# Kernel tuning notes

Measured on AMD Instinct MI355X. Metric: run time of the kernel, lower is better.

## Reference

```python
import jax, jax.numpy as jnp
import numpy as np

N = 50000      # nodes
E = 800000     # edges (before self-loops)
IN = 256       # input_dim
H = 8          # heads (hard-coded in module)
C = 32         # hidden_dim per head
OUT = 64       # output_dim
NEG_SLOPE = 0.2  # PyG GATConv default leaky_relu slope


def setup_inputs() -> dict:
    key = jax.random.key(0)
    ks = jax.random.split(key, 8)
    x = jax.random.normal(ks[0], (N, IN), dtype=jnp.float32)
    edge_index = jax.random.randint(ks[1], (2, E), 0, N, dtype=jnp.int64)
    # GATConv params (concat=True -> out width H*C)
    W_gat = jax.random.normal(ks[2], (IN, H * C), dtype=jnp.float32) * (1.0 / np.sqrt(IN))
    att_src = jax.random.normal(ks[3], (1, H, C), dtype=jnp.float32) * (1.0 / np.sqrt(C))
    att_dst = jax.random.normal(ks[4], (1, H, C), dtype=jnp.float32) * (1.0 / np.sqrt(C))
    bias_gat = jnp.zeros((H * C,), dtype=jnp.float32)
    # final Linear
    W_lin = jax.random.normal(ks[5], (H * C, OUT), dtype=jnp.float32) * (1.0 / np.sqrt(H * C))
    b_lin = jnp.zeros((OUT,), dtype=jnp.float32)
    return {"x": x, "edge_index": edge_index, "W_gat": W_gat, "att_src": att_src,
            "att_dst": att_dst, "bias_gat": bias_gat, "W_lin": W_lin, "b_lin": b_lin}


def reference(x, edge_index, W_gat, att_src, att_dst, bias_gat, W_lin, b_lin):
    # add self-loops (PyG GATConv default add_self_loops=True)
    ar = jnp.arange(N, dtype=edge_index.dtype)
    ei = jnp.concatenate([edge_index, jnp.stack([ar, ar])], axis=1)  # [2, E+N]
    src, dst = ei[0], ei[1]

    h = (x @ W_gat).reshape(N, H, C)                # [N,H,C]
    a_src = jnp.sum(h * att_src, axis=-1)           # [N,H]
    a_dst = jnp.sum(h * att_dst, axis=-1)           # [N,H]

    e = a_src[src] + a_dst[dst]                     # [E+N,H] per-edge logits
    e = jnp.where(e > 0, e, NEG_SLOPE * e)          # leaky_relu

    # segment softmax over incoming edges of each dst node
    m = jax.ops.segment_max(e, dst, num_segments=N)           # [N,H]
    ex = jnp.exp(e - m[dst])                                   # [E+N,H]
    denom = jax.ops.segment_sum(ex, dst, num_segments=N)       # [N,H]
    alpha = ex / (denom[dst] + 1e-16)                           # [E+N,H]

    msg = h[src] * alpha[:, :, None]                            # [E+N,H,C]
    out = jax.ops.segment_sum(msg, dst, num_segments=N)        # [N,H,C]
    out = out.reshape(N, H * C) + bias_gat                      # concat heads + bias

    out = jax.nn.relu(out)
    return out @ W_lin + b_lin                                  # [N,OUT]
```

## Files before the change

### kernel.cpp

```cpp
#include <hip/hip_runtime.h>
#include <hip/hip_bf16.h>

typedef __attribute__((ext_vector_type(8))) short short8v;
typedef __attribute__((ext_vector_type(4))) float floatx4;

__device__ __forceinline__ unsigned short f2bf(float f) {
    unsigned b = __float_as_uint(f);
    b = (b + 0x7fffu + ((b >> 16) & 1u)) >> 16;
    return (unsigned short)b;
}
__device__ __forceinline__ float b2f(unsigned short u) {
    return __uint_as_float((unsigned)u << 16);
}

#define BIDX(col, k) ((col) * 264 + ((k) ^ ((((col) >> 3) & 7) << 3)))

__global__ void k_prep(const float* __restrict__ s0, unsigned short* __restrict__ d0, int n0,
                       const float* __restrict__ s1, unsigned short* __restrict__ d1, int n1,
                       const float* __restrict__ s2, unsigned short* __restrict__ d2, int n2,
                       const int* __restrict__ ei, int* __restrict__ cnt, int E, int EE) {
    int nconv = n0 + n1 + n2;
    int total = nconv + EE;
    int i = blockIdx.x * blockDim.x + threadIdx.x;
    int stride = gridDim.x * blockDim.x;
    for (; i < total; i += stride) {
        if (i < nconv) {
            const float* s; unsigned short* d; int j;
            if (i < n0) { s = s0; d = d0; j = i; }
            else if (i < n0 + n1) { s = s1; d = d1; j = i - n0; }
            else { s = s2; d = d2; j = i - n0 - n1; }
            float4 v = reinterpret_cast<const float4*>(s)[j];
            ushort4 o;
            o.x = f2bf(v.x); o.y = f2bf(v.y); o.z = f2bf(v.z); o.w = f2bf(v.w);
            reinterpret_cast<ushort4*>(d)[j] = o;
        } else {
            int e = i - nconv;
            int dst = (e < E) ? ei[E + e] : e - E;
            atomicAdd(&cnt[dst], 1);
        }
    }
}

__launch_bounds__(256)
__global__ void k_gs(const unsigned short* __restrict__ A,
                     const unsigned short* __restrict__ B,
                     const float* __restrict__ att_src, const float* __restrict__ att_dst,
                     unsigned short* __restrict__ hb,
                     float* __restrict__ a_src, float* __restrict__ a_dst,
                     int M, int RB, int GB1,
                     const int* __restrict__ ei, int* __restrict__ cursor,
                     int* __restrict__ sorted_src, int E, int EE) {
    __shared__ unsigned short BsT[64 * 264];
    const int b = blockIdx.x;
    if (b >= GB1) {
        int e = (b - GB1) * 256 + threadIdx.x;
        if (e >= EE) return;
        int src, dst;
        if (e < E) { src = ei[e]; dst = ei[E + e]; } else { src = dst = e - E; }
        int pos = atomicAdd(&cursor[dst], 1);
        sorted_src[pos] = src;
        return;
    }
    const int tid = threadIdx.x;
    const int nt = b / RB;
    const int tM = (b - nt * RB) * 64;

    for (int it = 0; it < 8; ++it) {
        int f8 = it * 256 + tid;
        int k = f8 >> 3;
        int c0 = (f8 & 7) * 8;
        short8v v = *reinterpret_cast<const short8v*>(B + (size_t)k * 256 + nt * 64 + c0);
#pragma unroll
        for (int j = 0; j < 8; ++j)
            BsT[BIDX(c0 + j, k)] = (unsigned short)v[j];
    }
    __syncthreads();

    const int w  = tid >> 6;
    const int l  = tid & 63;
    const int lg = l >> 4;
    const int lr = l & 15;

    floatx4 acc[4] = {};
    int rowA = tM + w * 16 + lr;
    if (rowA > M - 1) rowA = M - 1;
    const unsigned short* Arow = A + (size_t)rowA * 256 + lg * 8;

#pragma unroll
    for (int kt = 0; kt < 8; ++kt) {
        short8v av = *reinterpret_cast<const short8v*>(Arow + kt * 32);
#pragma unroll
        for (int n = 0; n < 4; ++n) {
            short8v bv = *reinterpret_cast<const short8v*>(&BsT[BIDX(n * 16 + lr, kt * 32 + lg * 8)]);
            acc[n] = __builtin_amdgcn_mfma_f32_16x16x32_bf16(av, bv, acc[n], 0, 0, 0);
        }
    }

    float ps[2][4] = {}, pd[2][4] = {};
#pragma unroll
    for (int n = 0; n < 4; ++n) {
        int hd2 = n >> 1;
        float asv = att_src[(nt * 2 + hd2) * 32 + (n & 1) * 16 + lr];
        float adv = att_dst[(nt * 2 + hd2) * 32 + (n & 1) * 16 + lr];
        int col = nt * 64 + n * 16 + lr;
#pragma unroll
        for (int r = 0; r < 4; ++r) {
            int row = tM + w * 16 + lg * 4 + r;
            float v = acc[n][r];
            if (row < M) hb[(size_t)row * 256 + col] = f2bf(v);
            ps[hd2][r] += v * asv;
            pd[hd2][r] += v * adv;
        }
    }
#pragma unroll
    for (int off = 1; off < 16; off <<= 1) {
#pragma unroll
        for (int hd2 = 0; hd2 < 2; ++hd2)
#pragma unroll
            for (int r = 0; r < 4; ++r) {
                ps[hd2][r] += __shfl_xor(ps[hd2][r], off, 64);
                pd[hd2][r] += __shfl_xor(pd[hd2][r], off, 64);
            }
    }
    if (lr == 0) {
#pragma unroll
        for (int hd2 = 0; hd2 < 2; ++hd2)
#pragma unroll
            for (int r = 0; r < 4; ++r) {
                int row = tM + w * 16 + lg * 4 + r;
                if (row < M) {
                    a_src[(size_t)row * 8 + nt * 2 + hd2] = ps[hd2][r];
                    a_dst[(size_t)row * 8 + nt * 2 + hd2] = pd[hd2][r];
                }
            }
    }
}

__launch_bounds__(256)
__global__ void k_gemm(const unsigned short* __restrict__ A,
                       const unsigned short* __restrict__ B,
                       float* __restrict__ C,
                       const float* __restrict__ bias,
                       int M, int NC) {
    __shared__ unsigned short BsT[64 * 264];
    const int tid = threadIdx.x;
    const int ntile = blockIdx.y;
    const int tM = blockIdx.x * 64;

    for (int it = 0; it < 8; ++it) {
        int f8 = it * 256 + tid;
        int k = f8 >> 3;
        int c0 = (f8 & 7) * 8;
        short8v v = *reinterpret_cast<const short8v*>(B + (size_t)k * NC + ntile * 64 + c0);
#pragma unroll
        for (int j = 0; j < 8; ++j)
            BsT[BIDX(c0 + j, k)] = (unsigned short)v[j];
    }
    __syncthreads();

    const int w  = tid >> 6;
    const int l  = tid & 63;
    const int lg = l >> 4;
    const int lr = l & 15;

    floatx4 acc[4] = {};
    int rowA = tM + w * 16 + lr;
    if (rowA > M - 1) rowA = M - 1;
    const unsigned short* Arow = A + (size_t)rowA * 256 + lg * 8;

#pragma unroll
    for (int kt = 0; kt < 8; ++kt) {
        short8v av = *reinterpret_cast<const short8v*>(Arow + kt * 32);
#pragma unroll
        for (int n = 0; n < 4; ++n) {
            short8v bv = *reinterpret_cast<const short8v*>(&BsT[BIDX(n * 16 + lr, kt * 32 + lg * 8)]);
            acc[n] = __builtin_amdgcn_mfma_f32_16x16x32_bf16(av, bv, acc[n], 0, 0, 0);
        }
    }
#pragma unroll
    for (int n = 0; n < 4; ++n) {
        int col = ntile * 64 + n * 16 + lr;
        float badd = bias ? bias[col] : 0.0f;
#pragma unroll
        for (int r = 0; r < 4; ++r) {
            int row = tM + w * 16 + lg * 4 + r;
            if (row < M) C[(size_t)row * NC + col] = acc[n][r] + badd;
        }
    }
}

#define SCAN_NB 256
__launch_bounds__(256)
__global__ void k_scan_a(const int* __restrict__ cnt, int* __restrict__ bsum, int N) {
    __shared__ int sh[256];
    int b = blockIdx.x, t = threadIdx.x;
    int chunk = (N + SCAN_NB - 1) / SCAN_NB;
    int idx = b * chunk + t;
    sh[t] = (t < chunk && idx < N) ? cnt[idx] : 0;
    __syncthreads();
    for (int off = 128; off > 0; off >>= 1) {
        if (t < off) sh[t] += sh[t + off];
        __syncthreads();
    }
    if (t == 0) bsum[b] = sh[0];
}
__launch_bounds__(256)
__global__ void k_scan_bc(const int* __restrict__ cnt, const int* __restrict__ bsum,
                          int* __restrict__ row_start, int* __restrict__ cursor, int N) {
    __shared__ int shb[256];
    __shared__ int sh[256];
    int b = blockIdx.x, t = threadIdx.x;
    shb[t] = bsum[t];
    __syncthreads();
    for (int off = 1; off < 256; off <<= 1) {
        int v = (t >= off) ? shb[t - off] : 0;
        __syncthreads();
        shb[t] += v;
        __syncthreads();
    }
    int boff = (b == 0) ? 0 : shb[b - 1];

    int chunk = (N + SCAN_NB - 1) / SCAN_NB;
    int idx = b * chunk + t;
    int v = (t < chunk && idx < N) ? cnt[idx] : 0;
    sh[t] = v;
    __syncthreads();
    for (int off = 1; off < 256; off <<= 1) {
        int u = (t >= off) ? sh[t - off] : 0;
        __syncthreads();
        sh[t] += u;
        __syncthreads();
    }
    if (t < chunk && idx < N) {
        int ex = boff + sh[t] - v;
        row_start[idx] = ex;
        cursor[idx] = ex;
    }
}

__launch_bounds__(256)
__global__ void k_agg(const int* __restrict__ row_start, const int* __restrict__ row_end,
                      const int* __restrict__ sorted_src,
                      const float* __restrict__ a_src, const float* __restrict__ a_dst,
                      const unsigned short* __restrict__ hb,
                      const float* __restrict__ bias_gat,
                      unsigned short* __restrict__ gb, int N) {
    int n = blockIdx.x * 4 + (threadIdx.x >> 6);
    if (n >= N) return;
    int lane = threadIdx.x & 63;
    int hd = lane >> 3;
    int start = row_start[n], end = row_end[n];
    float ad = a_dst[(size_t)n * 8 + hd];
    float ax = 0.f, ay = 0.f, az = 0.f, aw = 0.f, den = 0.f;
    float bx = 0.f, by = 0.f, bz = 0.f, bw = 0.f, den2 = 0.f;
    for (int j0 = start; j0 < end; j0 += 64) {
        int idx = j0 + lane;
        int sv = (idx < end) ? sorted_src[idx] : 0;
        int cnt = end - j0; if (cnt > 64) cnt = 64;
        int jj = 0;
        for (; jj + 3 < cnt; jj += 4) {
            int s0 = __shfl(sv, jj);
            int s1 = __shfl(sv, jj + 1);
            int s2 = __shfl(sv, jj + 2);
            int s3 = __shfl(sv, jj + 3);
            float v0 = a_src[(size_t)s0 * 8 + hd] + ad;
            float v1 = a_src[(size_t)s1 * 8 + hd] + ad;
            float v2 = a_src[(size_t)s2 * 8 + hd] + ad;
            float v3 = a_src[(size_t)s3 * 8 + hd] + ad;
            ushort4 h0 = *reinterpret_cast<const ushort4*>(hb + (size_t)s0 * 256 + lane * 4);
            ushort4 h1 = *reinterpret_cast<const ushort4*>(hb + (size_t)s1 * 256 + lane * 4);
            ushort4 h2 = *reinterpret_cast<const ushort4*>(hb + (size_t)s2 * 256 + lane * 4);
            ushort4 h3 = *reinterpret_cast<const ushort4*>(hb + (size_t)s3 * 256 + lane * 4);
            v0 = v0 > 0.f ? v0 : 0.2f * v0;
            v1 = v1 > 0.f ? v1 : 0.2f * v1;
            v2 = v2 > 0.f ? v2 : 0.2f * v2;
            v3 = v3 > 0.f ? v3 : 0.2f * v3;
            float e0 = __expf(v0), e1 = __expf(v1), e2 = __expf(v2), e3 = __expf(v3);
            den  += e0 + e2; den2 += e1 + e3;
            ax += e0 * b2f(h0.x); ay += e0 * b2f(h0.y);
            az += e0 * b2f(h0.z); aw += e0 * b2f(h0.w);
            bx += e1 * b2f(h1.x); by += e1 * b2f(h1.y);
            bz += e1 * b2f(h1.z); bw += e1 * b2f(h1.w);
            ax += e2 * b2f(h2.x); ay += e2 * b2f(h2.y);
            az += e2 * b2f(h2.z); aw += e2 * b2f(h2.w);
            bx += e3 * b2f(h3.x); by += e3 * b2f(h3.y);
            bz += e3 * b2f(h3.z); bw += e3 * b2f(h3.w);
        }
        for (; jj < cnt; ++jj) {
            int s0 = __shfl(sv, jj);
            float v0 = a_src[(size_t)s0 * 8 + hd] + ad;
            v0 = v0 > 0.f ? v0 : 0.2f * v0;
            float e0 = __expf(v0);
            ushort4 h0 = *reinterpret_cast<const ushort4*>(hb + (size_t)s0 * 256 + lane * 4);
            den += e0;
            ax += e0 * b2f(h0.x); ay += e0 * b2f(h0.y);
            az += e0 * b2f(h0.z); aw += e0 * b2f(h0.w);
        }
    }
    float inv = 1.0f / (den + den2 + 1e-16f);
    float4 b4 = *reinterpret_cast<const float4*>(bias_gat + lane * 4);
    ushort4 o;
    o.x = f2bf(fmaxf((ax + bx) * inv + b4.x, 0.f));
    o.y = f2bf(fmaxf((ay + by) * inv + b4.y, 0.f));
    o.z = f2bf(fmaxf((az + bz) * inv + b4.z, 0.f));
    o.w = f2bf(fmaxf((aw + bw) * inv + b4.w, 0.f));
    reinterpret_cast<ushort4*>(gb)[(size_t)n * 64 + lane] = o;
}

extern "C" void kernel_launch(void* const* d_in, const int* in_sizes, int n_in,
                              void* d_out, int out_size, void* d_ws, size_t ws_size,
                              hipStream_t stream) {
    const float* x        = (const float*)d_in[0];
    const int*   ei       = (const int*)d_in[1];
    const float* W_gat    = (const float*)d_in[2];
    const float* att_src  = (const float*)d_in[3];
    const float* att_dst  = (const float*)d_in[4];
    const float* bias_gat = (const float*)d_in[5];
    const float* W_lin    = (const float*)d_in[6];
    const float* b_lin    = (const float*)d_in[7];
    float* out = (float*)d_out;

    const int N  = in_sizes[0] / 256;
    const int E  = in_sizes[1] / 2;
    const int EE = E + N;

    char* ws = (char*)d_ws;
    size_t off = 0;
    auto alloc = [&](size_t bytes) -> void* {
        void* p = ws + off;
        off = (off + bytes + 255) & ~(size_t)255;
        return p;
    };
    unsigned short* hb       = (unsigned short*)alloc((size_t)N * 256 * 2);
    float*          a_srcv   = (float*)alloc((size_t)N * 8 * 4);
    float*          a_dstv   = (float*)alloc((size_t)N * 8 * 4);
    int*            cnt      = (int*)alloc((size_t)N * 4);
    int*            rowst    = (int*)alloc((size_t)N * 4);
    int*            cursor   = (int*)alloc((size_t)N * 4);
    int*            bsum     = (int*)alloc(SCAN_NB * 4);
    int*            ssrc     = (int*)alloc((size_t)EE * 4);
    unsigned short* xb       = (unsigned short*)alloc((size_t)N * 256 * 2);
    unsigned short* wb       = (unsigned short*)alloc(256 * 256 * 2);
    unsigned short* wlb      = (unsigned short*)alloc(256 * 64 * 2);

    hipMemsetAsync(cnt, 0, (size_t)N * 4, stream);

    k_prep<<<2048, 256, 0, stream>>>(x, xb, N * 256 / 4,
                                     W_gat, wb, 256 * 256 / 4,
                                     W_lin, wlb, 256 * 64 / 4,
                                     ei, cnt, E, EE);

    k_scan_a<<<SCAN_NB, 256, 0, stream>>>(cnt, bsum, N);
    k_scan_bc<<<SCAN_NB, 256, 0, stream>>>(cnt, bsum, rowst, cursor, N);

    const int RB  = (N + 63) / 64;
    const int GB1 = RB * 4;
    const int SB  = (EE + 255) / 256;
    k_gs<<<GB1 + SB, 256, 0, stream>>>(xb, wb, att_src, att_dst, hb, a_srcv, a_dstv,
                                       N, RB, GB1, ei, cursor, ssrc, E, EE);

    k_agg<<<(N + 3) / 4, 256, 0, stream>>>(rowst, cursor, ssrc, a_srcv, a_dstv, hb,
                                           bias_gat, xb, N);

    dim3 g2((N + 63) / 64, 1);
    k_gemm<<<g2, 256, 0, stream>>>(xb, wlb, out, b_lin, N, 64);
}
```

Before: 220.4 us.

## Pre-transpose weights, drop LDS staging, compact edge indices to 16-bit

Weights are transposed to bf16 during the prep pass, so both GEMM kernels read B operands straight from global/L2 and no longer stage them through shared memory with a barrier. Self-loops are written directly during the scan instead of with atomics. Sorted source indices are stored as 16-bit values, halving that traffic, and the edge scatter handles four edges per thread with vector loads. The 16-bit indices only work because N is below 65536, and the uncoalesced transposed weight stores in prep add some cost.

```diff
diff --git a/kernel.cpp b/kernel.cpp
--- a/kernel.cpp
+++ b/kernel.cpp
@@ -13,86 +13,144 @@
     return __uint_as_float((unsigned)u << 16);
 }
 
-#define BIDX(col, k) ((col) * 264 + ((k) ^ ((((col) >> 3) & 7) << 3)))
-
-__global__ void k_prep(const float* __restrict__ s0, unsigned short* __restrict__ d0, int n0,
-                       const float* __restrict__ s1, unsigned short* __restrict__ d1, int n1,
-                       const float* __restrict__ s2, unsigned short* __restrict__ d2, int n2,
-                       const int* __restrict__ ei, int* __restrict__ cnt, int E, int EE) {
-    int nconv = n0 + n1 + n2;
-    int total = nconv + EE;
+__global__ void k_prep(const float* __restrict__ x, unsigned short* __restrict__ xb, int n0,
+                       const float* __restrict__ Wg, unsigned short* __restrict__ wbT,
+                       const float* __restrict__ Wl, unsigned short* __restrict__ wlbT,
+                       const int* __restrict__ ei, int* __restrict__ cnt, int E) {
+    const int TG = 256 * 256 / 4;
+    const int TL = 256 * 64 / 4;
+    int total = n0 + TG + TL + E;
     int i = blockIdx.x * blockDim.x + threadIdx.x;
     int stride = gridDim.x * blockDim.x;
     for (; i < total; i += stride) {
-        if (i < nconv) {
-            const float* s; unsigned short* d; int j;
-            if (i < n0) { s = s0; d = d0; j = i; }
-            else if (i < n0 + n1) { s = s1; d = d1; j = i - n0; }
-            else { s = s2; d = d2; j = i - n0 - n1; }
-            float4 v = reinterpret_cast<const float4*>(s)[j];
+        if (i < n0) {
+            float4 v = reinterpret_cast<const float4*>(x)[i];
             ushort4 o;
             o.x = f2bf(v.x); o.y = f2bf(v.y); o.z = f2bf(v.z); o.w = f2bf(v.w);
-            reinterpret_cast<ushort4*>(d)[j] = o;
+            reinterpret_cast<ushort4*>(xb)[i] = o;
+        } else if (i < n0 + TG) {
+            int j = i - n0;
+            int k = j >> 6, c4 = (j & 63) * 4;
+            float4 v = *reinterpret_cast<const float4*>(Wg + k * 256 + c4);
+            wbT[(size_t)(c4 + 0) * 256 + k] = f2bf(v.x);
+            wbT[(size_t)(c4 + 1) * 256 + k] = f2bf(v.y);
+            wbT[(size_t)(c4 + 2) * 256 + k] = f2bf(v.z);
+            wbT[(size_t)(c4 + 3) * 256 + k] = f2bf(v.w);
+        } else if (i < n0 + TG + TL) {
+            int j = i - n0 - TG;
+            int k = j >> 4, c4 = (j & 15) * 4;
+            float4 v = *reinterpret_cast<const float4*>(Wl + k * 64 + c4);
+            wlbT[(size_t)(c4 + 0) * 256 + k] = f2bf(v.x);
+            wlbT[(size_t)(c4 + 1) * 256 + k] = f2bf(v.y);
+            wlbT[(size_t)(c4 + 2) * 256 + k] = f2bf(v.z);
+            wlbT[(size_t)(c4 + 3) * 256 + k] = f2bf(v.w);
         } else {
-            int e = i - nconv;
-            int dst = (e < E) ? ei[E + e] : e - E;
-            atomicAdd(&cnt[dst], 1);
-        }
+            int e = i - n0 - TG - TL;
+            atomicAdd(&cnt[ei[E + e]], 1);
+        }
+    }
+}
+
+#define SCAN_NB 256
+__launch_bounds__(256)
+__global__ void k_scan_a(const int* __restrict__ cnt, int* __restrict__ bsum, int N) {
+    __shared__ int sh[256];
+    int b = blockIdx.x, t = threadIdx.x;
+    int chunk = (N + SCAN_NB - 1) / SCAN_NB;
+    int idx = b * chunk + t;
+    sh[t] = (t < chunk && idx < N) ? (cnt[idx] + 1) : 0;
+    __syncthreads();
+    for (int off = 128; off > 0; off >>= 1) {
+        if (t < off) sh[t] += sh[t + off];
+        __syncthreads();
+    }
+    if (t == 0) bsum[b] = sh[0];
+}
+__launch_bounds__(256)
+__global__ void k_scan_bc(const int* __restrict__ cnt, const int* __restrict__ bsum,
+                          int* __restrict__ row_start, int* __restrict__ cursor,
+                          unsigned short* __restrict__ ssrc, int N) {
+    __shared__ int shb[256];
+    __shared__ int sh[256];
+    int b = blockIdx.x, t = threadIdx.x;
+    shb[t] = bsum[t];
+    __syncthreads();
+    for (int off = 1; off < 256; off <<= 1) {
+        int v = (t >= off) ? shb[t - off] : 0;
+        __syncthreads();
+        shb[t] += v;
+        __syncthreads();
+    }
+    int boff = (b == 0) ? 0 : shb[b - 1];
+
+    int chunk = (N + SCAN_NB - 1) / SCAN_NB;
+    int idx = b * chunk + t;
+    int v = (t < chunk && idx < N) ? (cnt[idx] + 1) : 0;
+    sh[t] = v;
+    __syncthreads();
+    for (int off = 1; off < 256; off <<= 1) {
+        int u = (t >= off) ? sh[t - off] : 0;
+        __syncthreads();
+        sh[t] += u;
+        __syncthreads();
+    }
+    if (t < chunk && idx < N) {
+        int ex = boff + sh[t] - v;
+        row_start[idx] = ex;
+        cursor[idx] = ex + 1;
+        ssrc[ex] = (unsigned short)idx;
     }
 }
 
 __launch_bounds__(256)
 __global__ void k_gs(const unsigned short* __restrict__ A,
-                     const unsigned short* __restrict__ B,
+                     const unsigned short* __restrict__ BT,
                      const float* __restrict__ att_src, const float* __restrict__ att_dst,
                      unsigned short* __restrict__ hb,
                      float* __restrict__ a_src, float* __restrict__ a_dst,
                      int M, int RB, int GB1,
                      const int* __restrict__ ei, int* __restrict__ cursor,
-                     int* __restrict__ sorted_src, int E, int EE) {
-    __shared__ unsigned short BsT[64 * 264];
+                     unsigned short* __restrict__ ssrc, int E) {
     const int b = blockIdx.x;
+    const int tid = threadIdx.x;
     if (b >= GB1) {
-        int e = (b - GB1) * 256 + threadIdx.x;
-        if (e >= EE) return;
-        int src, dst;
-        if (e < E) { src = ei[e]; dst = ei[E + e]; } else { src = dst = e - E; }
-        int pos = atomicAdd(&cursor[dst], 1);
-        sorted_src[pos] = src;
+        int e0 = ((b - GB1) * 256 + tid) * 4;
+        if (e0 >= E) return;
+        int4 s4 = *reinterpret_cast<const int4*>(ei + e0);
+        int4 d4 = *reinterpret_cast<const int4*>(ei + E + e0);
+        int p0 = atomicAdd(&cursor[d4.x], 1);
+        int p1 = atomicAdd(&cursor[d4.y], 1);
+        int p2 = atomicAdd(&cursor[d4.z], 1);
+        int p3 = atomicAdd(&cursor[d4.w], 1);
+        ssrc[p0] = (unsigned short)s4.x;
+        ssrc[p1] = (unsigned short)s4.y;
+        ssrc[p2] = (unsigned short)s4.z;
+        ssrc[p3] = (unsigned short)s4.w;
         return;
     }
-    const int tid = threadIdx.x;
     const int nt = b / RB;
     const int tM = (b - nt * RB) * 64;
-
-    for (int it = 0; it < 8; ++it) {
-        int f8 = it * 256 + tid;
-        int k = f8 >> 3;
-        int c0 = (f8 & 7) * 8;
-        short8v v = *reinterpret_cast<const short8v*>(B + (size_t)k * 256 + nt * 64 + c0);
-#pragma unroll
-        for (int j = 0; j < 8; ++j)
-            BsT[BIDX(c0 + j, k)] = (unsigned short)v[j];
-    }
-    __syncthreads();
-
     const int w  = tid >> 6;
     const int l  = tid & 63;
     const int lg = l >> 4;
     const int lr = l & 15;
 
-    floatx4 acc[4] = {};
     int rowA = tM + w * 16 + lr;
     if (rowA > M - 1) rowA = M - 1;
     const unsigned short* Arow = A + (size_t)rowA * 256 + lg * 8;
-
+    short8v av[8];
+#pragma unroll
+    for (int kt = 0; kt < 8; ++kt)
+        av[kt] = *reinterpret_cast<const short8v*>(Arow + kt * 32);
+
+    const unsigned short* Bt = BT + (size_t)(nt * 64) * 256 + lg * 8;
+    floatx4 acc[4] = {};
 #pragma unroll
     for (int kt = 0; kt < 8; ++kt) {
-        short8v av = *reinterpret_cast<const short8v*>(Arow + kt * 32);
 #pragma unroll
         for (int n = 0; n < 4; ++n) {
-            short8v bv = *reinterpret_cast<const short8v*>(&BsT[BIDX(n * 16 + lr, kt * 32 + lg * 8)]);
-            acc[n] = __builtin_amdgcn_mfma_f32_16x16x32_bf16(av, bv, acc[n], 0, 0, 0);
+            short8v bv = *reinterpret_cast<const short8v*>(Bt + (size_t)(n * 16 + lr) * 256 + kt * 32);
+            acc[n] = __builtin_amdgcn_mfma_f32_16x16x32_bf16(av[kt], bv, acc[n], 0, 0, 0);
         }
     }
 
@@ -137,110 +195,47 @@
 }
 
 __launch_bounds__(256)
-__global__ void k_gemm(const unsigned short* __restrict__ A,
-                       const unsigned short* __restrict__ B,
-                       float* __restrict__ C,
-                       const float* __restrict__ bias,
-                       int M, int NC) {
-    __shared__ unsigned short BsT[64 * 264];
+__global__ void k_gemm2(const unsigned short* __restrict__ A,
+                        const unsigned short* __restrict__ BT,
+                        float* __restrict__ C,
+                        const float* __restrict__ bias, int M) {
     const int tid = threadIdx.x;
-    const int ntile = blockIdx.y;
     const int tM = blockIdx.x * 64;
-
-    for (int it = 0; it < 8; ++it) {
-        int f8 = it * 256 + tid;
-        int k = f8 >> 3;
-        int c0 = (f8 & 7) * 8;
-        short8v v = *reinterpret_cast<const short8v*>(B + (size_t)k * NC + ntile * 64 + c0);
-#pragma unroll
-        for (int j = 0; j < 8; ++j)
-            BsT[BIDX(c0 + j, k)] = (unsigned short)v[j];
-    }
-    __syncthreads();
-
     const int w  = tid >> 6;
     const int l  = tid & 63;
     const int lg = l >> 4;
     const int lr = l & 15;
 
-    floatx4 acc[4] = {};
     int rowA = tM + w * 16 + lr;
     if (rowA > M - 1) rowA = M - 1;
     const unsigned short* Arow = A + (size_t)rowA * 256 + lg * 8;
-
+    const unsigned short* Bt = BT + lg * 8;
+
+    floatx4 acc[4] = {};
 #pragma unroll
     for (int kt = 0; kt < 8; ++kt) {
         short8v av = *reinterpret_cast<const short8v*>(Arow + kt * 32);
 #pragma unroll
         for (int n = 0; n < 4; ++n) {
-            short8v bv = *reinterpret_cast<const short8v*>(&BsT[BIDX(n * 16 + lr, kt * 32 + lg * 8)]);
+            short8v bv = *reinterpret_cast<const short8v*>(Bt + (size_t)(n * 16 + lr) * 256 + kt * 32);
             acc[n] = __builtin_amdgcn_mfma_f32_16x16x32_bf16(av, bv, acc[n], 0, 0, 0);
         }
     }
 #pragma unroll
     for (int n = 0; n < 4; ++n) {
-        int col = ntile * 64 + n * 16 + lr;
-        float badd = bias ? bias[col] : 0.0f;
+        int col = n * 16 + lr;
+        float badd = bias[col];
 #pragma unroll
         for (int r = 0; r < 4; ++r) {
             int row = tM + w * 16 + lg * 4 + r;
-            if (row < M) C[(size_t)row * NC + col] = acc[n][r] + badd;
-        }
-    }
-}
-
-#define SCAN_NB 256
-__launch_bounds__(256)
-__global__ void k_scan_a(const int* __restrict__ cnt, int* __restrict__ bsum, int N) {
-    __shared__ int sh[256];
-    int b = blockIdx.x, t = threadIdx.x;
-    int chunk = (N + SCAN_NB - 1) / SCAN_NB;
-    int idx = b * chunk + t;
-    sh[t] = (t < chunk && idx < N) ? cnt[idx] : 0;
-    __syncthreads();
-    for (int off = 128; off > 0; off >>= 1) {
-        if (t < off) sh[t] += sh[t + off];
-        __syncthreads();
-    }
-    if (t == 0) bsum[b] = sh[0];
-}
-__launch_bounds__(256)
-__global__ void k_scan_bc(const int* __restrict__ cnt, const int* __restrict__ bsum,
-                          int* __restrict__ row_start, int* __restrict__ cursor, int N) {
-    __shared__ int shb[256];
-    __shared__ int sh[256];
-    int b = blockIdx.x, t = threadIdx.x;
-    shb[t] = bsum[t];
-    __syncthreads();
-    for (int off = 1; off < 256; off <<= 1) {
-        int v = (t >= off) ? shb[t - off] : 0;
-        __syncthreads();
-        shb[t] += v;
-        __syncthreads();
-    }
-    int boff = (b == 0) ? 0 : shb[b - 1];
-
-    int chunk = (N + SCAN_NB - 1) / SCAN_NB;
-    int idx = b * chunk + t;
-    int v = (t < chunk && idx < N) ? cnt[idx] : 0;
-    sh[t] = v;
-    __syncthreads();
-    for (int off = 1; off < 256; off <<= 1) {
-        int u = (t >= off) ? sh[t - off] : 0;
-        __syncthreads();
-        sh[t] += u;
-        __syncthreads();
-    }
-    if (t < chunk && idx < N) {
-        int ex = boff + sh[t] - v;
-        row_start[idx] = ex;
-        cursor[idx] = ex;
+            if (row < M) C[(size_t)row * 64 + col] = acc[n][r] + badd;
+        }
     }
 }
 
 __launch_bounds__(256)
 __global__ void k_agg(const int* __restrict__ row_start, const int* __restrict__ row_end,
-                      const int* __restrict__ sorted_src,
+                      const unsigned short* __restrict__ sorted_src,
                       const float* __restrict__ a_src, const float* __restrict__ a_dst,
                       const unsigned short* __restrict__ hb,
                       const float* __restrict__ bias_gat,
@@ -255,7 +250,7 @@
     float bx = 0.f, by = 0.f, bz = 0.f, bw = 0.f, den2 = 0.f;
     for (int j0 = start; j0 < end; j0 += 64) {
         int idx = j0 + lane;
-        int sv = (idx < end) ? sorted_src[idx] : 0;
+        int sv = (idx < end) ? (int)sorted_src[idx] : 0;
         int cnt = end - j0; if (cnt > 64) cnt = 64;
         int jj = 0;
         for (; jj + 3 < cnt; jj += 4) {
@@ -338,30 +333,27 @@
     int*            rowst    = (int*)alloc((size_t)N * 4);
     int*            cursor   = (int*)alloc((size_t)N * 4);
     int*            bsum     = (int*)alloc(SCAN_NB * 4);
-    int*            ssrc     = (int*)alloc((size_t)EE * 4);
+    unsigned short* ssrc     = (unsigned short*)alloc((size_t)EE * 2);
     unsigned short* xb       = (unsigned short*)alloc((size_t)N * 256 * 2);
-    unsigned short* wb       = (unsigned short*)alloc(256 * 256 * 2);
-    unsigned short* wlb      = (unsigned short*)alloc(256 * 64 * 2);
+    unsigned short* wbT      = (unsigned short*)alloc(256 * 256 * 2);
+    unsigned short* wlbT     = (unsigned short*)alloc(64 * 256 * 2);
 
     hipMemsetAsync(cnt, 0, (size_t)N * 4, stream);
 
     k_prep<<<2048, 256, 0, stream>>>(x, xb, N * 256 / 4,
-                                     W_gat, wb, 256 * 256 / 4,
-                                     W_lin, wlb, 256 * 64 / 4,
-                                     ei, cnt, E, EE);
+                                     W_gat, wbT, W_lin, wlbT, ei, cnt, E);
 
     k_scan_a<<<SCAN_NB, 256, 0, stream>>>(cnt, bsum, N);
-    k_scan_bc<<<SCAN_NB, 256, 0, stream>>>(cnt, bsum, rowst, cursor, N);
+    k_scan_bc<<<SCAN_NB, 256, 0, stream>>>(cnt, bsum, rowst, cursor, ssrc, N);
 
     const int RB  = (N + 63) / 64;
     const int GB1 = RB * 4;
-    const int SB  = (EE + 255) / 256;
-    k_gs<<<GB1 + SB, 256, 0, stream>>>(xb, wb, att_src, att_dst, hb, a_srcv, a_dstv,
-                                       N, RB, GB1, ei, cursor, ssrc, E, EE);
+    const int SB  = (E / 4 + 255) / 256;
+    k_gs<<<GB1 + SB, 256, 0, stream>>>(xb, wbT, att_src, att_dst, hb, a_srcv, a_dstv,
+                                       N, RB, GB1, ei, cursor, ssrc, E);
 
     k_agg<<<(N + 3) / 4, 256, 0, stream>>>(rowst, cursor, ssrc, a_srcv, a_dstv, hb,
                                            bias_gat, xb, N);
 
-    dim3 g2((N + 63) / 64, 1);
-    k_gemm<<<g2, 256, 0, stream>>>(xb, wlb, out, b_lin, N, 64);
-}
+    k_gemm2<<<(N + 63) / 64, 256, 0, stream>>>(xb, wlbT, out, b_lin, N);
+}
```

New measurement: 250.3 us. 1.14x slower.
